# Optimization experiments

Hardware: AMD Instinct MI355X
Metric: run time of the kernel (lower is better)

## Reference

```python
import jax, jax.numpy as jnp
import numpy as np
from jax import lax

# Dimensions: wave-ordered clade DAG over gene families
N_LEAVES = 65536   # leaf clades (phase-0)
WAVES = 24         # number of topological waves
WC = 2048          # max_wave_size: internal clades per wave
K = 3              # CCP splits per internal clade
S = 128            # species-tree nodes
C = N_LEAVES + WAVES * WC   # total clades = 114688
G = 2048           # gene families
E_ITERS = 50       # fixed-point iterations for extinction solve (max_iters_E analog)
EPS = 1e-30


def setup_inputs() -> dict:
    key = jax.random.key(0)
    k0, k1, k2, k3, k4, k5 = jax.random.split(key, 6)
    return {
        "theta": jax.random.normal(k0, (3,), jnp.float32),
        "wave_split_logw": jax.random.normal(k1, (WAVES, WC, K), jnp.float32),
        "wave_left": jax.random.randint(k2, (WAVES, WC, K), 0, C, jnp.int32),
        "wave_right": jax.random.randint(k3, (WAVES, WC, K), 0, C, jnp.int32),
        "leaf_species": jax.random.randint(k4, (N_LEAVES,), 0, S, jnp.int32),
        "root_ids": jax.random.randint(k5, (G,), 0, C, jnp.int32),
    }


def reference(theta, wave_split_logw, wave_left, wave_right, leaf_species, root_ids):
    # theta holds log2(D, L, T) DTL rates (global mode)
    rates = jnp.exp2(theta)
    D, L, T = rates[0], rates[1], rates[2]
    norm = D + L + T + 1.0

    # Extinction probabilities e[s]: fixed-point iteration (fixed iters, jit/vjp-safe)
    def e_step(e, _):
        return (L + D * e * e + T * e.mean() * e) / norm, None
    e, _ = lax.scan(e_step, jnp.full((S,), L / norm, jnp.float32), None, length=E_ITERS)
    denom = 1.0 + D * e + T * e.mean()   # [S] per-species survival normalizer

    # Leaf clades: one-hot on their observed species (leaf_row/col scatter)
    P = jnp.zeros((C, S), jnp.float32).at[jnp.arange(N_LEAVES), leaf_species].set(1.0)
    ls = jnp.zeros((C,), jnp.float32)    # per-clade log row-max scale (unnorm_row_max)

    def wave_step(carry, xs):
        P, ls = carry
        left, right, logw, k = xs
        Pl = P[left]   # [WC, K, S] gather of child-clade likelihood rows
        Pr = P[right]  # [WC, K, S]
        w = jax.nn.softmax(logw, axis=-1)[..., None]  # CCP split probabilities
        # uniform pibar: mean-excluding-self transfer donor term (pibar_mode='uniform')
        pib = lambda X: (X.sum(-1, keepdims=True) - X) / (S - 1)
        vals = (w * ((1.0 + D) * Pl * Pr + T * (Pl * pib(Pr) + Pr * pib(Pl)))).sum(1) / denom
        # row-max renormalization to prevent underflow, log-scale recorded per clade
        safe = jnp.maximum(vals.max(-1, keepdims=True), EPS)
        ids = N_LEAVES + k * WC + jnp.arange(WC)
        P = P.at[ids].set(vals / safe)
        ls = ls.at[ids].set(jnp.log(safe[:, 0]))
        return (P, ls), None

    (P, ls), _ = lax.scan(
        wave_step, (P, ls),
        (wave_left, wave_right, wave_split_logw, jnp.arange(WAVES)),
    )

    # Root clades: per-family log-likelihood, reduce='sum' -> scalar NLL
    ll = jnp.log(P[root_ids].sum(-1) + EPS) + ls[root_ids]
    return -ll.sum()
```

## Files before the change

kernel.cpp:

```cpp
#include <hip/hip_runtime.h>
#include <math.h>

#define N_LEAVES 65536
#define WAVES 24
#define WC 2048
#define KSPLITS 3
#define S 128
#define N_INT (WAVES * WC)
#define G 2048
#define E_ITERS 50
#define EPS 1e-30f

#define NBLK 768
#define TPB 512

#define AGENT __HIP_MEMORY_SCOPE_AGENT
#define SENT8 0xFFFFFFFFFFFFFFFFull
#define SENT4 0xFFFFFFFFu

union F2U { float2 f; unsigned long long u; };

__global__ __launch_bounds__(256) void init_kernel(uint4* __restrict__ P4,
                                                   unsigned long long* __restrict__ meta,
                                                   float* __restrict__ out) {
    const int NP4 = N_INT * S / 4;
    int idx = blockIdx.x * 256 + threadIdx.x;
    int stride = gridDim.x * 256;
    uint4 s4 = make_uint4(SENT4, SENT4, SENT4, SENT4);
    for (int i = idx; i < NP4; i += stride) P4[i] = s4;
    for (int i = idx; i < N_INT; i += stride) meta[i] = SENT8;
    if (idx == 0) out[0] = 0.0f;
}

__device__ __forceinline__ unsigned long long frag_load(const float* __restrict__ P,
                                                        int r, int lane) {
    return __hip_atomic_load((const unsigned long long*)(P + (size_t)r * S) + lane,
                             __ATOMIC_RELAXED, AGENT);
}
__device__ __forceinline__ float rsum_load(const unsigned long long* __restrict__ meta,
                                           int r) {
    unsigned u = __hip_atomic_load((const unsigned*)(meta + r), __ATOMIC_RELAXED, AGENT);
    return __uint_as_float(u);
}

#define SLOT_DECL(Sx)                                                          \
  float2 pv##Sx[6]; float rs##Sx[6]; float wq##Sx[3];                          \
  int pend##Sx = 0, base##Sx = 0;

#define REFILL(Sx, KK)                                                         \
  {                                                                            \
    const int kk_ = (KK);                                                      \
    if (kk_ < WAVES) {                                                         \
      const int b_ = (kk_ * WC + c) * KSPLITS;                                 \
      base##Sx = b_;                                                           \
      const int lo_ = N_LEAVES + kk_ * WC;                                     \
      float l0_ = logw[b_], l1_ = logw[b_ + 1], l2_ = logw[b_ + 2];            \
      float m_ = fmaxf(l0_, fmaxf(l1_, l2_));                                  \
      float e0_ = expf(l0_ - m_), e1_ = expf(l1_ - m_), e2_ = expf(l2_ - m_);  \
      float inv_ = 1.0f / (e0_ + e1_ + e2_);                                   \
      wq##Sx[0] = e0_ * inv_; wq##Sx[1] = e1_ * inv_; wq##Sx[2] = e2_ * inv_;  \
      pend##Sx = 0;                                                            \
      _Pragma("unroll")                                                        \
      for (int j_ = 0; j_ < 6; ++j_) {                                         \
        int idx_ = (j_ < 3) ? left[b_ + j_] : right[b_ + j_ - 3];              \
        float2 v_ = make_float2(0.f, 0.f);                                     \
        float rs_ = 0.f;                                                       \
        if (idx_ < N_LEAVES) {                                                 \
          int sp_ = leaf_species[idx_];                                        \
          v_.x = (sp_ == 2 * lane) ? 1.f : 0.f;                                \
          v_.y = (sp_ == 2 * lane + 1) ? 1.f : 0.f;                            \
          rs_ = 1.f;                                                           \
        } else if (idx_ < lo_) {                                               \
          pend##Sx |= 1 << j_;                                                 \
          int r_ = idx_ - N_LEAVES;                                            \
          F2U u_; u_.u = frag_load(P, r_, lane);                               \
          v_ = u_.f;                                                           \
          rs_ = rsum_load(meta, r_);                                           \
        }                                                                      \
        pv##Sx[j_] = v_; rs##Sx[j_] = rs_;                                     \
      }                                                                        \
    }                                                                          \
  }

#define RESOLVE_SPIN(Sx)                                                       \
  while (pend##Sx) {                                                           \
    int done_ = 0;                                                             \
    _Pragma("unroll")                                                          \
    for (int j_ = 0; j_ < 6; ++j_)                                             \
      if ((pend##Sx >> j_) & 1) {                                              \
        int idx_ = (j_ < 3) ? left[base##Sx + j_] : right[base##Sx + j_ - 3];  \
        int r_ = idx_ - N_LEAVES;                                              \
        F2U u_; u_.f = pv##Sx[j_];                                             \
        if (u_.u == SENT8) { u_.u = frag_load(P, r_, lane); pv##Sx[j_] = u_.f; } \
        if (__float_as_uint(rs##Sx[j_]) == SENT4)                              \
          rs##Sx[j_] = rsum_load(meta, r_);                                    \
        if (__all((u_.u != SENT8) && (__float_as_uint(rs##Sx[j_]) != SENT4)))  \
          done_ |= 1 << j_;                                                    \
      }                                                                        \
    pend##Sx &= ~done_;                                                        \
    if (pend##Sx) __builtin_amdgcn_s_sleep(1);                                 \
  }

#define FIRE(Sx, KK)                                                           \
  {                                                                            \
    float v0_ = 0.f, v1_ = 0.f;                                                \
    _Pragma("unroll")                                                          \
    for (int jj_ = 0; jj_ < KSPLITS; ++jj_) {                                  \
      float2 a_ = pv##Sx[jj_], b_ = pv##Sx[jj_ + 3];                           \
      float sl_ = rs##Sx[jj_], sr_ = rs##Sx[jj_ + 3], w_ = wq##Sx[jj_];        \
      v0_ += w_ * (onepD * a_.x * b_.x +                                       \
                   T127 * (a_.x * (sr_ - b_.x) + b_.x * (sl_ - a_.x)));        \
      v1_ += w_ * (onepD * a_.y * b_.y +                                       \
                   T127 * (a_.y * (sr_ - b_.y) + b_.y * (sl_ - a_.y)));        \
    }                                                                          \
    v0_ /= denom; v1_ /= denom;                                                \
    float mx_ = fmaxf(v0_, v1_);                                               \
    float tt_ = v0_ + v1_;                                                     \
    _Pragma("unroll")                                                          \
    for (int d_ = 1; d_ < 64; d_ <<= 1) {                                      \
      mx_ = fmaxf(mx_, __shfl_xor(mx_, d_));                                   \
      tt_ += __shfl_xor(tt_, d_);                                              \
    }                                                                          \
    const float safe_ = fmaxf(mx_, EPS);                                       \
    const int row_ = (KK) * WC + c;                                            \
    F2U o_; o_.f = make_float2(v0_ / safe_, v1_ / safe_);                      \
    __hip_atomic_store((unsigned long long*)(P + (size_t)row_ * S) + lane,     \
                       o_.u, __ATOMIC_RELAXED, AGENT);                         \
    if (lane == 0) {                                                           \
      F2U mo_; mo_.f = make_float2(tt_ / safe_, logf(safe_));                  \
      __hip_atomic_store(&meta[row_], mo_.u, __ATOMIC_RELAXED, AGENT);         \
    }                                                                          \
  }

__global__ __launch_bounds__(TPB, 6) void fused_kernel(
    const float* __restrict__ theta, const float* __restrict__ logw,
    const int* __restrict__ left, const int* __restrict__ right,
    const int* __restrict__ leaf_species, const int* __restrict__ root_ids,
    float* __restrict__ P, unsigned long long* __restrict__ meta,
    float* __restrict__ out) {
    const int lane = threadIdx.x & 63;
    const int w = blockIdx.x * (TPB / 64) + (threadIdx.x >> 6);
    const int c = w / 3;
    const int q = w - 3 * c;

    const float D = exp2f(theta[0]);
    const float L = exp2f(theta[1]);
    const float T = exp2f(theta[2]);
    const float norm = D + L + T + 1.0f;
    float e = L / norm;
#pragma unroll 1
    for (int i = 0; i < E_ITERS; ++i)
        e = (L + D * e * e + T * e * e) / norm;
    const float denom = 1.0f + D * e + T * e;
    const float onepD = 1.0f + D;
    const float T127 = T / 127.0f;

    SLOT_DECL(A) SLOT_DECL(B)

    REFILL(A, q) REFILL(B, q + 3)

#pragma unroll 1
    for (int k = q; k < WAVES; k += 6) {
        RESOLVE_SPIN(A) FIRE(A, k)     REFILL(A, k + 6)
        RESOLVE_SPIN(B) FIRE(B, k + 3) REFILL(B, k + 9)
    }

    const int r = root_ids[c];
    if (q == 0 && r >= N_LEAVES && lane == 0) {
        const int row = r - N_LEAVES;
        F2U m;
        while ((m.u = __hip_atomic_load(&meta[row], __ATOMIC_RELAXED, AGENT)) == SENT8)
            __builtin_amdgcn_s_sleep(1);
        atomicAdd(out, -(logf(m.f.x + EPS) + m.f.y));
    }
}

extern "C" void kernel_launch(void* const* d_in, const int* in_sizes, int n_in,
                              void* d_out, int out_size, void* d_ws, size_t ws_size,
                              hipStream_t stream) {
    const float* theta        = (const float*)d_in[0];
    const float* logw         = (const float*)d_in[1];
    const int*   left         = (const int*)d_in[2];
    const int*   right        = (const int*)d_in[3];
    const int*   leaf_species = (const int*)d_in[4];
    const int*   root_ids     = (const int*)d_in[5];
    float* out = (float*)d_out;

    char* ws = (char*)d_ws;
    float* P = (float*)ws;
    unsigned long long* meta =
        (unsigned long long*)(ws + (size_t)N_INT * S * 4);

    init_kernel<<<2048, 256, 0, stream>>>((uint4*)P, meta, out);
    fused_kernel<<<NBLK, TPB, 0, stream>>>(theta, logw, left, right,
                                           leaf_species, root_ids,
                                           P, meta, out);
}
```

Before: 73.59 us.

## Replace per-element sentinel polling with meta-flag publish and dependent row gather

Stops pre-filling the whole P buffer with sentinels; only the per-row meta word acts as a ready flag. The producer waits for its row stores to complete (s_waitcnt) before publishing meta, and consumers poll meta first and then gather the row with an address-dependent load. Child index, species and meta loads are batched up front in REFILL to overlap latency, and the spin sleep is lengthened. This removes roughly 24 MB of init writes and per-element sentinel checks, at the cost of relying on relaxed-ordering tricks (vmcnt wait plus a fake address dependency) for correctness across workgroups.

```diff
diff --git a/kernel.cpp b/kernel.cpp
--- a/kernel.cpp
+++ b/kernel.cpp
@@ -16,31 +16,27 @@
 
 #define AGENT __HIP_MEMORY_SCOPE_AGENT
 #define SENT8 0xFFFFFFFFFFFFFFFFull
-#define SENT4 0xFFFFFFFFu
 
 union F2U { float2 f; unsigned long long u; };
 
-__global__ __launch_bounds__(256) void init_kernel(uint4* __restrict__ P4,
-                                                   unsigned long long* __restrict__ meta,
+__global__ __launch_bounds__(256) void init_kernel(unsigned long long* __restrict__ meta,
                                                    float* __restrict__ out) {
-    const int NP4 = N_INT * S / 4;
-    int idx = blockIdx.x * 256 + threadIdx.x;
-    int stride = gridDim.x * 256;
-    uint4 s4 = make_uint4(SENT4, SENT4, SENT4, SENT4);
-    for (int i = idx; i < NP4; i += stride) P4[i] = s4;
-    for (int i = idx; i < N_INT; i += stride) meta[i] = SENT8;
-    if (idx == 0) out[0] = 0.0f;
-}
-
-__device__ __forceinline__ unsigned long long frag_load(const float* __restrict__ P,
-                                                        int r, int lane) {
-    return __hip_atomic_load((const unsigned long long*)(P + (size_t)r * S) + lane,
-                             __ATOMIC_RELAXED, AGENT);
-}
-__device__ __forceinline__ float rsum_load(const unsigned long long* __restrict__ meta,
-                                           int r) {
-    unsigned u = __hip_atomic_load((const unsigned*)(meta + r), __ATOMIC_RELAXED, AGENT);
-    return __uint_as_float(u);
+    int i = blockIdx.x * 256 + threadIdx.x;
+    if (i < N_INT) meta[i] = SENT8;
+    if (i == 0) out[0] = 0.0f;
+}
+
+__device__ __forceinline__ unsigned long long meta_load(
+    const unsigned long long* __restrict__ meta, int r) {
+    return __hip_atomic_load(meta + r, __ATOMIC_RELAXED, AGENT);
+}
+__device__ __forceinline__ float2 row_gather(const float* __restrict__ P,
+                                             int r, int lane, int dep) {
+    F2U x;
+    x.u = __hip_atomic_load(
+        (const unsigned long long*)(P + (size_t)r * S) + (lane + dep),
+        __ATOMIC_RELAXED, AGENT);
+    return x.f;
 }
 
 #define SLOT_DECL(Sx)                                                          \
@@ -59,23 +55,36 @@
       float e0_ = expf(l0_ - m_), e1_ = expf(l1_ - m_), e2_ = expf(l2_ - m_);  \
       float inv_ = 1.0f / (e0_ + e1_ + e2_);                                   \
       wq##Sx[0] = e0_ * inv_; wq##Sx[1] = e1_ * inv_; wq##Sx[2] = e2_ * inv_;  \
+      int idxv_[6]; int spv_[6]; unsigned long long mu_[6];                    \
+      _Pragma("unroll")                                                        \
+      for (int j_ = 0; j_ < 6; ++j_) {                                         \
+        int idx_ = (j_ < 3) ? left[b_ + j_] : right[b_ + j_ - 3];              \
+        idxv_[j_] = idx_;                                                      \
+        int sidx_ = idx_ < N_LEAVES ? idx_ : 0;                                \
+        spv_[j_] = leaf_species[sidx_];                                        \
+        int rr_ = idx_ - N_LEAVES;                                             \
+        rr_ = rr_ < 0 ? 0 : (rr_ >= N_INT ? N_INT - 1 : rr_);                  \
+        mu_[j_] = meta_load(meta, rr_);                                        \
+      }                                                                        \
       pend##Sx = 0;                                                            \
       _Pragma("unroll")                                                        \
       for (int j_ = 0; j_ < 6; ++j_) {                                         \
-        int idx_ = (j_ < 3) ? left[b_ + j_] : right[b_ + j_ - 3];              \
+        int idx_ = idxv_[j_];                                                  \
         float2 v_ = make_float2(0.f, 0.f);                                     \
         float rs_ = 0.f;                                                       \
         if (idx_ < N_LEAVES) {                                                 \
-          int sp_ = leaf_species[idx_];                                        \
-          v_.x = (sp_ == 2 * lane) ? 1.f : 0.f;                                \
-          v_.y = (sp_ == 2 * lane + 1) ? 1.f : 0.f;                            \
+          v_.x = (spv_[j_] == 2 * lane) ? 1.f : 0.f;                           \
+          v_.y = (spv_[j_] == 2 * lane + 1) ? 1.f : 0.f;                       \
           rs_ = 1.f;                                                           \
         } else if (idx_ < lo_) {                                               \
-          pend##Sx |= 1 << j_;                                                 \
-          int r_ = idx_ - N_LEAVES;                                            \
-          F2U u_; u_.u = frag_load(P, r_, lane);                               \
-          v_ = u_.f;                                                           \
-          rs_ = rsum_load(meta, r_);                                           \
+          if (__all(mu_[j_] != SENT8)) {                                       \
+            F2U mm_; mm_.u = mu_[j_];                                          \
+            rs_ = mm_.f.x;                                                     \
+            v_ = row_gather(P, idx_ - N_LEAVES, lane,                          \
+                            (int)(mu_[j_] == SENT8));                          \
+          } else {                                                             \
+            pend##Sx |= 1 << j_;                                               \
+          }                                                                    \
         }                                                                      \
         pv##Sx[j_] = v_; rs##Sx[j_] = rs_;                                     \
       }                                                                        \
@@ -89,16 +98,17 @@
     for (int j_ = 0; j_ < 6; ++j_)                                             \
       if ((pend##Sx >> j_) & 1) {                                              \
         int idx_ = (j_ < 3) ? left[base##Sx + j_] : right[base##Sx + j_ - 3];  \
-        int r_ = idx_ - N_LEAVES;                                              \
-        F2U u_; u_.f = pv##Sx[j_];                                             \
-        if (u_.u == SENT8) { u_.u = frag_load(P, r_, lane); pv##Sx[j_] = u_.f; } \
-        if (__float_as_uint(rs##Sx[j_]) == SENT4)                              \
-          rs##Sx[j_] = rsum_load(meta, r_);                                    \
-        if (__all((u_.u != SENT8) && (__float_as_uint(rs##Sx[j_]) != SENT4)))  \
+        int rr_ = idx_ - N_LEAVES;                                             \
+        unsigned long long mu_ = meta_load(meta, rr_);                         \
+        if (__all(mu_ != SENT8)) {                                             \
+          F2U mm_; mm_.u = mu_;                                                \
+          rs##Sx[j_] = mm_.f.x;                                                \
+          pv##Sx[j_] = row_gather(P, rr_, lane, (int)(mu_ == SENT8));          \
           done_ |= 1 << j_;                                                    \
+        }                                                                      \
       }                                                                        \
     pend##Sx &= ~done_;                                                        \
-    if (pend##Sx) __builtin_amdgcn_s_sleep(1);                                 \
+    if (pend##Sx) __builtin_amdgcn_s_sleep(2);                                 \
   }
 
 #define FIRE(Sx, KK)                                                           \
@@ -126,6 +136,7 @@
     F2U o_; o_.f = make_float2(v0_ / safe_, v1_ / safe_);                      \
     __hip_atomic_store((unsigned long long*)(P + (size_t)row_ * S) + lane,     \
                        o_.u, __ATOMIC_RELAXED, AGENT);                         \
+    asm volatile("s_waitcnt vmcnt(0)" ::: "memory");                           \
     if (lane == 0) {                                                           \
       F2U mo_; mo_.f = make_float2(tt_ / safe_, logf(safe_));                  \
       __hip_atomic_store(&meta[row_], mo_.u, __ATOMIC_RELAXED, AGENT);         \
@@ -170,7 +181,7 @@
         const int row = r - N_LEAVES;
         F2U m;
         while ((m.u = __hip_atomic_load(&meta[row], __ATOMIC_RELAXED, AGENT)) == SENT8)
-            __builtin_amdgcn_s_sleep(1);
+            __builtin_amdgcn_s_sleep(2);
         atomicAdd(out, -(logf(m.f.x + EPS) + m.f.y));
     }
 }
@@ -191,7 +202,7 @@
     unsigned long long* meta =
         (unsigned long long*)(ws + (size_t)N_INT * S * 4);
 
-    init_kernel<<<2048, 256, 0, stream>>>((uint4*)P, meta, out);
+    init_kernel<<<(N_INT + 255) / 256, 256, 0, stream>>>(meta, out);
     fused_kernel<<<NBLK, TPB, 0, stream>>>(theta, logw, left, right,
                                            leaf_species, root_ids,
                                            P, meta, out);
```

After: 65.02 us. -11.6%, faster.
